# Kernel tuning notes

Hardware: AMD Instinct MI355X
Metric: run time of the kernel (lower is better)

The kernel has to match this reference:

```python
import jax, jax.numpy as jnp
import numpy as np

B, C, H, W = 256, 3, 256, 256
ROT_DEG = 180.0
COLOR = 0.3
CROP = 256


def _sample_bilinear(img, ix, iy, zeros_pad):
    # img: [B,C,H,W]; ix, iy: [B,Ho,Wo] pixel-space coords
    Hh, Ww = img.shape[2], img.shape[3]
    x0 = jnp.floor(ix)
    y0 = jnp.floor(iy)
    wx = ix - x0
    wy = iy - y0

    def gather(yy, xx):
        yc = jnp.clip(yy, 0, Hh - 1).astype(jnp.int32)
        xc = jnp.clip(xx, 0, Ww - 1).astype(jnp.int32)
        v = jax.vmap(lambda im, y, x: im[:, y, x])(img, yc, xc)  # [B,C,Ho,Wo]
        if zeros_pad:  # torch grid_sample padding_mode='zeros': zero each OOB corner
            valid = ((yy >= 0) & (yy <= Hh - 1) & (xx >= 0) & (xx <= Ww - 1))
            v = v * valid[:, None].astype(img.dtype)
        return v

    return (gather(y0, x0) * ((1 - wy) * (1 - wx))[:, None]
            + gather(y0, x0 + 1) * ((1 - wy) * wx)[:, None]
            + gather(y0 + 1, x0) * (wy * (1 - wx))[:, None]
            + gather(y0 + 1, x0 + 1) * (wy * wx)[:, None])


def setup_inputs() -> dict:
    key = jax.random.key(0)
    ks = jax.random.split(key, 8)
    return {
        'images': jax.random.normal(ks[0], (B, C, H, W), dtype=jnp.float32),
        'rand_theta': jax.random.uniform(ks[1], (B,), dtype=jnp.float32),
        'rand_flip': jax.random.uniform(ks[2], (B,), dtype=jnp.float32),
        'rand_sizes': jax.random.uniform(ks[3], (B, 2), dtype=jnp.float32),
        'rand_shifts': jax.random.uniform(ks[4], (B, 2), dtype=jnp.float32),
        'rand_delta': jax.random.uniform(ks[5], (B, 1, 1, 1), dtype=jnp.float32),
        'rand_mag1': jax.random.uniform(ks[6], (B, 1, 1, 1), dtype=jnp.float32),
        'rand_mag2': jax.random.uniform(ks[7], (B, 1, 1, 1), dtype=jnp.float32),
    }


def reference(images, rand_theta, rand_flip, rand_sizes, rand_shifts,
              rand_delta, rand_mag1, rand_mag2):
    b, c, h, w = images.shape
    dt = images.dtype

    # ---- per-sample rotation: affine_grid + grid_sample (align_corners=False, zeros pad)
    theta = (rand_theta * 2 - 1) * (ROT_DEG * np.pi / 180.0)
    cth, sth = jnp.cos(theta), jnp.sin(theta)  # G_inv = rotate2d(theta)
    xn = (2 * jnp.arange(w, dtype=dt) + 1) / w - 1  # [W] normalized coords
    yn = (2 * jnp.arange(h, dtype=dt) + 1) / h - 1  # [H]
    xg = xn[None, None, :]
    yg = yn[None, :, None]
    xp = cth[:, None, None] * xg - sth[:, None, None] * yg  # [B,H,W]
    yp = sth[:, None, None] * xg + cth[:, None, None] * yg
    ix = ((xp + 1) * w - 1) / 2
    iy = ((yp + 1) * h - 1) / 2
    images = _sample_bilinear(images, ix, iy, zeros_pad=True)

    # ---- random horizontal flip
    flip = rand_flip > 0.5
    images = jnp.where(flip[:, None, None, None], images[..., ::-1], images)

    # ---- per-sample zoom (bilinear resize, align_corners=True) + shifted center crop
    sizes = jnp.round(h * (rand_sizes / 4 + 1.0) - 0.5)  # [B,2], values in [256, 320]
    max_shifts = sizes - CROP
    shift_ranges = max_shifts - 1e-5
    shifts = jnp.round(rand_shifts * shift_ranges - shift_ranges / 2)
    start = jnp.floor(max_shifts / 2) + shifts  # crop start (sh, sw), [B,2]
    ys = jnp.arange(h, dtype=dt)
    xs = jnp.arange(w, dtype=dt)
    # crop pixel (y,x) in the resized image maps to source coord via align_corners=True
    sy = (start[:, 0:1] + ys[None, :]) * (h - 1) / (sizes[:, 0:1] - 1)  # [B,H]
    sx = (start[:, 1:2] + xs[None, :]) * (w - 1) / (sizes[:, 1:2] - 1)  # [B,W]
    sy = jnp.clip(sy, 0, h - 1)
    sx = jnp.clip(sx, 0, w - 1)
    iy2 = jnp.broadcast_to(sy[:, :, None], (b, h, w))
    ix2 = jnp.broadcast_to(sx[:, None, :], (b, h, w))
    images = _sample_bilinear(images, ix2, iy2, zeros_pad=False)

    # ---- color jitter chain
    delta = (rand_delta * 2 - 1) * COLOR
    images = images + delta
    mag1 = (rand_mag1 * 2 - 1) * COLOR + 1
    x_mean = images.mean(axis=1, keepdims=True)
    images = (images - x_mean) * mag1 + x_mean
    mag2 = (rand_mag2 * 2 - 1) * COLOR + 1
    x_mean = images.mean(axis=(1, 2, 3), keepdims=True)
    images = (images - x_mean) * mag2 + x_mean
    return images
```

## Files before the change

kernel.cpp:

```cpp
#include <hip/hip_runtime.h>
#include <math.h>

#define Bn 256
#define Cc 3
#define Hh 256
#define Ww 256
#define HW (Hh*Ww)
#define CHW (Cc*HW)

#define P_BASE 256
#define P_STRIDE 10

#define TS 16
#define RY 29
#define RXS 33
#define PLANE1 (RY*RXS)
#define N1 (Cc*PLANE1)
#define S2 18
#define S2S 20
#define PLANE2 (S2*S2S)

__global__ void setup_params(const float* __restrict__ th, const float* __restrict__ fl,
                             const float* __restrict__ sz, const float* __restrict__ sh,
                             const float* __restrict__ de, const float* __restrict__ m1,
                             const float* __restrict__ m2, float* __restrict__ ws) {
    int b = threadIdx.x;
    ws[b] = 0.0f;
    float* p = ws + P_BASE + b * P_STRIDE;
    float theta = (th[b] * 2.0f - 1.0f) * 3.14159265358979323846f;
    p[0] = cosf(theta);
    p[1] = sinf(theta);
    p[2] = (fl[b] > 0.5f) ? 1.0f : 0.0f;
    #pragma unroll
    for (int d = 0; d < 2; d++) {
        float s     = rintf(256.0f * (sz[b*2 + d] * 0.25f + 1.0f) - 0.5f);
        float ms    = s - 256.0f;
        float sr    = ms - 1e-5f;
        float shf   = rintf(sh[b*2 + d] * sr - sr * 0.5f);
        float start = floorf(ms * 0.5f) + shf;
        p[3 + 2*d]  = start;
        p[4 + 2*d]  = 255.0f / (s - 1.0f);
    }
    p[7] = (de[b] * 2.0f - 1.0f) * 0.3f;
    p[8] = (m1[b] * 2.0f - 1.0f) * 0.3f + 1.0f;
    p[9] = (m2[b] * 2.0f - 1.0f) * 0.3f + 1.0f;
}

__global__ __launch_bounds__(256)
void augment_main(const float* __restrict__ img, const float* __restrict__ wsp,
                  float* __restrict__ out, float* __restrict__ sums) {
    __shared__ float L1[N1];
    __shared__ float L2[Cc*PLANE2];
    __shared__ float wred[4];

    const int tid = threadIdx.x;

    const int lin = blockIdx.x + (blockIdx.y << 4) + (blockIdx.z << 8);
    const int nid = (lin & 7) * (65536 / 8) + (lin >> 3);
    const int b     = nid >> 8;
    const int tileY = ((nid >> 4) & 15) << 4;
    const int tileX = (nid & 15) << 4;

    const float* p = wsp + P_BASE + b * P_STRIDE;
    const float cth = p[0], sth = p[1];
    const bool  flip = p[2] > 0.5f;
    const float startY = p[3], scaleY = p[4];
    const float startX = p[5], scaleX = p[6];
    const float delta = p[7], mag1 = p[8];

    float sy0 = fminf(fmaxf((startY + (float)tileY) * scaleY, 0.0f), 255.0f);
    float sx0 = fminf(fmaxf((startX + (float)tileX) * scaleX, 0.0f), 255.0f);
    const int rY = (int)floorf(sy0);
    const int rX = (int)floorf(sx0);

    const int Ymax = min(rY + S2 - 1, 255);
    const int Xt1  = min(rX + S2 - 1, 255);
    const int Xf0  = flip ? 255 - Xt1 : rX;
    const int Xf1  = flip ? 255 - rX  : Xt1;
    const float xg0 = fmaf((float)Xf0, 0.0078125f, -0.99609375f);
    const float xg1 = fmaf((float)Xf1, 0.0078125f, -0.99609375f);
    const float yg0 = fmaf((float)rY,  0.0078125f, -0.99609375f);
    const float yg1 = fmaf((float)Ymax,0.0078125f, -0.99609375f);

    float ixmin = 1e30f, iymin = 1e30f;
    #pragma unroll
    for (int cy = 0; cy < 2; cy++) {
        #pragma unroll
        for (int cx = 0; cx < 2; cx++) {
            float xg = cx ? xg1 : xg0;
            float yg = cy ? yg1 : yg0;
            float xp = cth * xg - sth * yg;
            float yp = sth * xg + cth * yg;
            ixmin = fminf(ixmin, fmaf(xp, 128.0f, 127.5f));
            iymin = fminf(iymin, fmaf(yp, 128.0f, 127.5f));
        }
    }
    const int bx0 = (int)floorf(ixmin) - 1;
    const int by0 = (int)floorf(iymin) - 1;
    const int bx0a = bx0 & ~3;

    const float* imgb = img + (size_t)b * CHW;
    {
        const int r  = tid >> 3;
        const int c4 = (tid & 7) << 2;
        if (r < RY) {
            const int ry = min(max(by0 + r, 0), 255);
            const float* srow = imgb + (ry << 8);
            float* drow = L1 + r * RXS + c4;
            if (bx0a >= 0 && bx0a <= 224) {
                const float* s0 = srow + bx0a + c4;
                #pragma unroll
                for (int ch = 0; ch < Cc; ch++) {
                    float4 v = *(const float4*)(s0 + (ch << 16));
                    float* d = drow + ch * PLANE1;
                    d[0] = v.x; d[1] = v.y; d[2] = v.z; d[3] = v.w;
                }
            } else {
                #pragma unroll
                for (int j = 0; j < 4; j++) {
                    int gx = min(max(bx0a + c4 + j, 0), 255);
                    #pragma unroll
                    for (int ch = 0; ch < Cc; ch++)
                        drow[ch * PLANE1 + j] = srow[(ch << 16) + gx];
                }
            }
        }
    }
    __syncthreads();

    for (int i = tid; i < S2 * S2; i += 256) {
        int lY = i / S2;
        int lX = i - lY * S2;
        int Yc = min(rY + lY, 255);
        int Xc = min(rX + lX, 255);
        int Xf = flip ? 255 - Xc : Xc;
        float xg = fmaf((float)Xf, 0.0078125f, -0.99609375f);
        float yg = fmaf((float)Yc, 0.0078125f, -0.99609375f);
        float xp = cth * xg - sth * yg;
        float yp = sth * xg + cth * yg;
        float ixf = fmaf(xp, 128.0f, 127.5f);
        float iyf = fmaf(yp, 128.0f, 127.5f);
        float x0f = floorf(ixf), y0f = floorf(iyf);
        float fx = ixf - x0f, fy = iyf - y0f;
        float wx0 = (x0f >=  0.0f && x0f <= 255.0f) ? (1.0f - fx) : 0.0f;
        float wx1 = (x0f >= -1.0f && x0f <= 254.0f) ? fx          : 0.0f;
        float wy0 = (y0f >=  0.0f && y0f <= 255.0f) ? (1.0f - fy) : 0.0f;
        float wy1 = (y0f >= -1.0f && y0f <= 254.0f) ? fy          : 0.0f;
        int ax = (int)x0f - bx0a;
        int ay = (int)y0f - by0;
        int ib = ay * RXS + ax;
        float w00 = wy0 * wx0, w01 = wy0 * wx1, w10 = wy1 * wx0, w11 = wy1 * wx1;
        int ob = lY * S2S + lX;
        #pragma unroll
        for (int c = 0; c < Cc; c++) {
            const float* Lc = L1 + c * PLANE1;
            float v = w00 * Lc[ib]       + w01 * Lc[ib + 1]
                    + w10 * Lc[ib + RXS] + w11 * Lc[ib + RXS + 1];
            L2[c * PLANE2 + ob] = v;
        }
    }
    __syncthreads();

    const int py = tid >> 4, px = tid & 15;
    const int y = tileY + py, x = tileX + px;
    float sy = fminf(fmaxf((startY + (float)y) * scaleY, 0.0f), 255.0f);
    float sx = fminf(fmaxf((startX + (float)x) * scaleX, 0.0f), 255.0f);
    float y0f = floorf(sy), x0f = floorf(sx);
    float fy = sy - y0f, fx = sx - x0f;
    int ly = (int)y0f - rY;
    int lx = (int)x0f - rX;
    int ib2 = ly * S2S + lx;
    float w00 = (1.0f - fy) * (1.0f - fx), w01 = (1.0f - fy) * fx;
    float w10 = fy * (1.0f - fx),          w11 = fy * fx;

    float x4[3];
    #pragma unroll
    for (int c = 0; c < Cc; c++) {
        const float* Lc = L2 + c * PLANE2;
        float v = w00 * Lc[ib2]       + w01 * Lc[ib2 + 1]
                + w10 * Lc[ib2 + S2S] + w11 * Lc[ib2 + S2S + 1];
        x4[c] = v + delta;
    }
    float mc = (x4[0] + x4[1] + x4[2]) * (1.0f/3.0f);
    float s5 = 0.0f;
    float* outb = out + (size_t)b * CHW + (y << 8) + x;
    #pragma unroll
    for (int c = 0; c < Cc; c++) {
        float v5 = (x4[c] - mc) * mag1 + mc;
        outb[c * HW] = v5;
        s5 += v5;
    }
    #pragma unroll
    for (int off = 32; off > 0; off >>= 1) s5 += __shfl_down(s5, off, 64);
    int lane = tid & 63, wid = tid >> 6;
    if (lane == 0) wred[wid] = s5;
    __syncthreads();
    if (tid == 0) atomicAdd(&sums[b], wred[0] + wred[1] + wred[2] + wred[3]);
}

__global__ __launch_bounds__(256)
void finalize_k(float* __restrict__ out, const float* __restrict__ wsp) {
    const int b = blockIdx.y;
    const float m    = wsp[b] * (1.0f / (float)CHW);
    const float mag2 = wsp[P_BASE + b * P_STRIDE + 9];
    float4* ob = (float4*)(out + (size_t)b * CHW);
    int idx = blockIdx.x * 256 + threadIdx.x;
    float4 v = ob[idx];
    v.x = (v.x - m) * mag2 + m;
    v.y = (v.y - m) * mag2 + m;
    v.z = (v.z - m) * mag2 + m;
    v.w = (v.w - m) * mag2 + m;
    ob[idx] = v;
}

extern "C" void kernel_launch(void* const* d_in, const int* in_sizes, int n_in,
                              void* d_out, int out_size, void* d_ws, size_t ws_size,
                              hipStream_t stream) {
    const float* img = (const float*)d_in[0];
    const float* th  = (const float*)d_in[1];
    const float* fl  = (const float*)d_in[2];
    const float* sz  = (const float*)d_in[3];
    const float* sh  = (const float*)d_in[4];
    const float* de  = (const float*)d_in[5];
    const float* m1  = (const float*)d_in[6];
    const float* m2  = (const float*)d_in[7];
    float* out = (float*)d_out;
    float* ws  = (float*)d_ws;

    hipLaunchKernelGGL(setup_params, dim3(1), dim3(256), 0, stream,
                       th, fl, sz, sh, de, m1, m2, ws);
    hipLaunchKernelGGL(augment_main, dim3(Ww/TS, Hh/TS, Bn), dim3(256), 0, stream,
                       img, ws, out, ws);
    hipLaunchKernelGGL(finalize_k, dim3(CHW/4/256, Bn), dim3(256), 0, stream,
                       out, ws);
}
```

Baseline: 463.2 us.

## Trim LDS patch loads, mirror patch for negative-shear rotations, specialize interior tiles

The change loads only the rows and columns of the rotated source patch that the tile actually needs, rather than the full 29x33 window. For rotations where cos*sin is negative it stores the patch mirrored horizontally in LDS, and it specializes the rotation-sampling loop for tiles that lie fully inside the image, which removes the out-of-bounds weight checks. The color-jitter arithmetic is folded into a single FMA per channel. These aim to cut global loads, LDS bank conflicts and ALU work, at the cost of four code-path variants and more branch divergence across blocks.

```diff
diff --git a/kernel.cpp b/kernel.cpp
--- a/kernel.cpp
+++ b/kernel.cpp
@@ -46,6 +46,47 @@
     p[9] = (m2[b] * 2.0f - 1.0f) * 0.3f + 1.0f;
 }
 
+#define PHASE_B_LOOP(MIR, INTR)                                               \
+    for (int i = tid; i < S2 * S2; i += 256) {                                \
+        int lY = i / S2;                                                      \
+        int lX = i - lY * S2;                                                 \
+        int Yc = min(rY + lY, 255);                                           \
+        int Xc = min(rX + lX, 255);                                           \
+        int Xf = flip ? 255 - Xc : Xc;                                        \
+        float xg = fmaf((float)Xf, 0.0078125f, -0.99609375f);                 \
+        float yg = fmaf((float)Yc, 0.0078125f, -0.99609375f);                 \
+        float xp = cth * xg - sth * yg;                                       \
+        float yp = sth * xg + cth * yg;                                       \
+        float ixf = fmaf(xp, 128.0f, 127.5f);                                 \
+        float iyf = fmaf(yp, 128.0f, 127.5f);                                 \
+        float x0f = floorf(ixf), y0f = floorf(iyf);                           \
+        float fx = ixf - x0f, fy = iyf - y0f;                                 \
+        float wx0, wx1, wy0, wy1;                                             \
+        if (INTR) {                                                           \
+            wx0 = 1.0f - fx; wx1 = fx; wy0 = 1.0f - fy; wy1 = fy;             \
+        } else {                                                              \
+            wx0 = (x0f >=  0.0f && x0f <= 255.0f) ? (1.0f - fx) : 0.0f;       \
+            wx1 = (x0f >= -1.0f && x0f <= 254.0f) ? fx          : 0.0f;       \
+            wy0 = (y0f >=  0.0f && y0f <= 255.0f) ? (1.0f - fy) : 0.0f;       \
+            wy1 = (y0f >= -1.0f && y0f <= 254.0f) ? fy          : 0.0f;       \
+        }                                                                     \
+        int ax = (int)x0f - bx0a;              \
+        int ay = (int)y0f - by0;                               \
+        int base = ay * RXS + (MIR ? (30 - ax) : ax);                         \
+        float A0 = MIR ? wx1 : wx0;                 \
+        float A1 = MIR ? wx0 : wx1;                                           \
+        float w00 = wy0 * A0, w01 = wy0 * A1;                                 \
+        float w10 = wy1 * A0, w11 = wy1 * A1;                                 \
+        int ob = lY * S2S + lX;                                               \
+        _Pragma("unroll")                                                     \
+        for (int c = 0; c < Cc; c++) {                                        \
+            const float* Lc = L1 + c * PLANE1;                                \
+            float v = w00 * Lc[base]       + w01 * Lc[base + 1]               \
+                    + w10 * Lc[base + RXS] + w11 * Lc[base + RXS + 1];        \
+            L2[c * PLANE2 + ob] = v;                                          \
+        }                                                                     \
+    }
+
 __global__ __launch_bounds__(256)
 void augment_main(const float* __restrict__ img, const float* __restrict__ wsp,
                   float* __restrict__ out, float* __restrict__ sums) {
@@ -67,6 +108,7 @@
     const float startY = p[3], scaleY = p[4];
     const float startX = p[5], scaleX = p[6];
     const float delta = p[7], mag1 = p[8];
+    const bool mir = (cth * sth) < 0.0f;
 
     float sy0 = fminf(fmaxf((startY + (float)tileY) * scaleY, 0.0f), 255.0f);
     float sx0 = fminf(fmaxf((startX + (float)tileX) * scaleX, 0.0f), 255.0f);
@@ -82,7 +124,7 @@
     const float yg0 = fmaf((float)rY,  0.0078125f, -0.99609375f);
     const float yg1 = fmaf((float)Ymax,0.0078125f, -0.99609375f);
 
-    float ixmin = 1e30f, iymin = 1e30f;
+    float ixmin = 1e30f, iymin = 1e30f, ixmax = -1e30f, iymax = -1e30f;
     #pragma unroll
     for (int cy = 0; cy < 2; cy++) {
         #pragma unroll
@@ -91,73 +133,64 @@
             float yg = cy ? yg1 : yg0;
             float xp = cth * xg - sth * yg;
             float yp = sth * xg + cth * yg;
-            ixmin = fminf(ixmin, fmaf(xp, 128.0f, 127.5f));
-            iymin = fminf(iymin, fmaf(yp, 128.0f, 127.5f));
+            float tx = fmaf(xp, 128.0f, 127.5f);
+            float ty = fmaf(yp, 128.0f, 127.5f);
+            ixmin = fminf(ixmin, tx); ixmax = fmaxf(ixmax, tx);
+            iymin = fminf(iymin, ty); iymax = fmaxf(iymax, ty);
         }
     }
     const int bx0 = (int)floorf(ixmin) - 1;
     const int by0 = (int)floorf(iymin) - 1;
     const int bx0a = bx0 & ~3;
+    const int rneed = min(RY, (int)floorf(iymax) - by0 + 2);
+    const int cneed = (int)floorf(ixmax) - bx0a + 2;
+    const bool interior = (ixmin >= 0.0f) && (iymin >= 0.0f) &&
+                          (ixmax < 255.0f) && (iymax < 255.0f);
 
     const float* imgb = img + (size_t)b * CHW;
     {
         const int r  = tid >> 3;
         const int c4 = (tid & 7) << 2;
-        if (r < RY) {
+        if (r < rneed && c4 < cneed) {
             const int ry = min(max(by0 + r, 0), 255);
             const float* srow = imgb + (ry << 8);
-            float* drow = L1 + r * RXS + c4;
             if (bx0a >= 0 && bx0a <= 224) {
                 const float* s0 = srow + bx0a + c4;
-                #pragma unroll
-                for (int ch = 0; ch < Cc; ch++) {
-                    float4 v = *(const float4*)(s0 + (ch << 16));
-                    float* d = drow + ch * PLANE1;
-                    d[0] = v.x; d[1] = v.y; d[2] = v.z; d[3] = v.w;
+                if (!mir) {
+                    float* d = L1 + r * RXS + c4;
+                    #pragma unroll
+                    for (int ch = 0; ch < Cc; ch++) {
+                        float4 v = *(const float4*)(s0 + (ch << 16));
+                        float* dd = d + ch * PLANE1;
+                        dd[0] = v.x; dd[1] = v.y; dd[2] = v.z; dd[3] = v.w;
+                    }
+                } else {
+                    float* d = L1 + r * RXS + (28 - c4);
+                    #pragma unroll
+                    for (int ch = 0; ch < Cc; ch++) {
+                        float4 v = *(const float4*)(s0 + (ch << 16));
+                        float* dd = d + ch * PLANE1;
+                        dd[0] = v.w; dd[1] = v.z; dd[2] = v.y; dd[3] = v.x;
+                    }
                 }
             } else {
                 #pragma unroll
                 for (int j = 0; j < 4; j++) {
                     int gx = min(max(bx0a + c4 + j, 0), 255);
+                    int sx = mir ? (31 - (c4 + j)) : (c4 + j);
                     #pragma unroll
                     for (int ch = 0; ch < Cc; ch++)
-                        drow[ch * PLANE1 + j] = srow[(ch << 16) + gx];
+                        L1[ch * PLANE1 + r * RXS + sx] = srow[(ch << 16) + gx];
                 }
             }
         }
     }
     __syncthreads();
 
-    for (int i = tid; i < S2 * S2; i += 256) {
-        int lY = i / S2;
-        int lX = i - lY * S2;
-        int Yc = min(rY + lY, 255);
-        int Xc = min(rX + lX, 255);
-        int Xf = flip ? 255 - Xc : Xc;
-        float xg = fmaf((float)Xf, 0.0078125f, -0.99609375f);
-        float yg = fmaf((float)Yc, 0.0078125f, -0.99609375f);
-        float xp = cth * xg - sth * yg;
-        float yp = sth * xg + cth * yg;
-        float ixf = fmaf(xp, 128.0f, 127.5f);
-        float iyf = fmaf(yp, 128.0f, 127.5f);
-        float x0f = floorf(ixf), y0f = floorf(iyf);
-        float fx = ixf - x0f, fy = iyf - y0f;
-        float wx0 = (x0f >=  0.0f && x0f <= 255.0f) ? (1.0f - fx) : 0.0f;
-        float wx1 = (x0f >= -1.0f && x0f <= 254.0f) ? fx          : 0.0f;
-        float wy0 = (y0f >=  0.0f && y0f <= 255.0f) ? (1.0f - fy) : 0.0f;
-        float wy1 = (y0f >= -1.0f && y0f <= 254.0f) ? fy          : 0.0f;
-        int ax = (int)x0f - bx0a;
-        int ay = (int)y0f - by0;
-        int ib = ay * RXS + ax;
-        float w00 = wy0 * wx0, w01 = wy0 * wx1, w10 = wy1 * wx0, w11 = wy1 * wx1;
-        int ob = lY * S2S + lX;
-        #pragma unroll
-        for (int c = 0; c < Cc; c++) {
-            const float* Lc = L1 + c * PLANE1;
-            float v = w00 * Lc[ib]       + w01 * Lc[ib + 1]
-                    + w10 * Lc[ib + RXS] + w11 * Lc[ib + RXS + 1];
-            L2[c * PLANE2 + ob] = v;
-        }
+    if (interior) {
+        if (mir) { PHASE_B_LOOP(true,  true) } else { PHASE_B_LOOP(false, true) }
+    } else {
+        if (mir) { PHASE_B_LOOP(true,  false) } else { PHASE_B_LOOP(false, false) }
     }
     __syncthreads();
 
@@ -173,20 +206,20 @@
     float w00 = (1.0f - fy) * (1.0f - fx), w01 = (1.0f - fy) * fx;
     float w10 = fy * (1.0f - fx),          w11 = fy * fx;
 
-    float x4[3];
+    float vv[3];
     #pragma unroll
     for (int c = 0; c < Cc; c++) {
         const float* Lc = L2 + c * PLANE2;
-        float v = w00 * Lc[ib2]       + w01 * Lc[ib2 + 1]
-                + w10 * Lc[ib2 + S2S] + w11 * Lc[ib2 + S2S + 1];
-        x4[c] = v + delta;
-    }
-    float mc = (x4[0] + x4[1] + x4[2]) * (1.0f/3.0f);
+        vv[c] = w00 * Lc[ib2]       + w01 * Lc[ib2 + 1]
+              + w10 * Lc[ib2 + S2S] + w11 * Lc[ib2 + S2S + 1];
+    }
+    float mc  = (vv[0] + vv[1] + vv[2]) * (1.0f/3.0f);
+    float mck = fmaf(-mag1, mc, mc) + delta;
     float s5 = 0.0f;
     float* outb = out + (size_t)b * CHW + (y << 8) + x;
     #pragma unroll
     for (int c = 0; c < Cc; c++) {
-        float v5 = (x4[c] - mc) * mag1 + mc;
+        float v5 = fmaf(vv[c], mag1, mck);
         outb[c * HW] = v5;
         s5 += v5;
     }
```

Measured after the change: 451.6 us. -2.5%, faster.
